# Performance work log

Measured on AMD Instinct MI355X. Metric: run time of the kernel, lower is better.

## Reference

```python
import jax, jax.numpy as jnp
import numpy as np

B, S, D_IN, D_OUT = 4, 2048, 1024, 1024

def setup_inputs() -> dict:
    key = jax.random.key(0)
    k1, k2, k3, k4 = jax.random.split(key, 4)
    sc = 0.02
    return {
        "x": jax.random.normal(k1, (B, S, D_IN), dtype=jnp.float32),
        "Wq": jax.random.normal(k2, (D_OUT, D_IN), dtype=jnp.float32) * sc,
        "Wk": jax.random.normal(k3, (D_OUT, D_IN), dtype=jnp.float32) * sc,
        "Wv": jax.random.normal(k4, (D_OUT, D_IN), dtype=jnp.float32) * sc,
    }

def reference(x, Wq, Wk, Wv):
    # torch Linear: y = x @ W.T  (weights stored [out, in])
    b, n, _ = x.shape
    q = jnp.einsum('bnd,od->bno', x, Wq)  # [B,S,D_OUT]
    k = jnp.einsum('bnd,od->bno', x, Wk)
    v = jnp.einsum('bnd,od->bno', x, Wv)
    scores = jnp.einsum('bqd,bkd->bqk', q, k)  # [B,S,S]
    # causal mask: positions j > i masked to -inf BEFORE scaling (matches source)
    causal = jnp.triu(jnp.ones((n, n), dtype=bool), k=1)
    scores = jnp.where(causal[None, :, :], -jnp.inf, scores)
    scale = 1.0 / jnp.sqrt(jnp.float32(k.shape[-1]))
    attn = jax.nn.softmax(scores * scale, axis=-1)
    # NOTE: source calls dropout but discards its output -> no-op
    return jnp.einsum('bqk,bkd->bqd', attn, v)
```

## Files before the change

### kernel.cpp

```cpp
#include <hip/hip_runtime.h>
#include <hip/hip_bf16.h>
#include <hip/hip_fp16.h>


using bf16 = __hip_bfloat16;
typedef __bf16 bf16x8 __attribute__((ext_vector_type(8)));
typedef float f32x4 __attribute__((ext_vector_type(4)));

__device__ __forceinline__ void load_lds_16B(const void* g, void* l) {
  __builtin_amdgcn_global_load_lds(
      (const __attribute__((address_space(1))) unsigned int*)g,
      (__attribute__((address_space(3))) unsigned int*)l, 16, 0, 0);
}

template <int N>
__device__ __forceinline__ void waitcnt_vm() {
  if constexpr (N == 8) asm volatile("s_waitcnt vmcnt(8)" ::: "memory");
  else if constexpr (N == 6) asm volatile("s_waitcnt vmcnt(6)" ::: "memory");
  else if constexpr (N == 4) asm volatile("s_waitcnt vmcnt(4)" ::: "memory");
  else if constexpr (N == 3) asm volatile("s_waitcnt vmcnt(3)" ::: "memory");
  else asm volatile("s_waitcnt vmcnt(0)" ::: "memory");
}

__device__ __forceinline__ int swz(int o) { return o ^ (((o >> 7) & 7) << 4); }

template <int M_REP, bool OUT_BF16, bool CSKIP, bool KLIM>
__global__ __launch_bounds__(512, 2) void gemm_pipe(
    const bf16* __restrict__ A, const bf16* __restrict__ Bm, void* __restrict__ Cv,
    int M, int N, int K, long sAz, long sBz, long sCzBytes) {
  constexpr int BM = M_REP * 32;
  constexpr int BN = 256;
  constexpr int ABYT = BM * 64;
  constexpr int BBYT = BN * 64;
  constexpr int NCALL = (ABYT + BBYT) / 8192;

  const int tn = blockIdx.x, tm = blockIdx.y, z = blockIdx.z;
  if (CSKIP && tn * BN >= tm * BM + BM) return;
  A += (long)z * sAz;
  Bm += (long)z * sBz;
  char* C = (char*)Cv + (long)z * sCzBytes;

  int kEnd = K;
  if (KLIM) kEnd = min(tm * BM + BM, K);
  const int nt = kEnd >> 5;

  __shared__ char sm[4 * (ABYT + BBYT)];

  const int tid = threadIdx.x;
  const int lane = tid & 63, wv = tid >> 6;
  const int wr = wv >> 2, wc = wv & 3;

  const char* srcp[NCALL];
  int ldsbase[NCALL];
  int bufstride[NCALL];
#pragma unroll
  for (int c = 0; c < NCALL; c++) {
    int oall = c * 8192 + tid * 16;
    int oc = c * 8192 + wv * 1024;
    bool isB = oall >= ABYT;
    int toff = isB ? (oall - ABYT) : oall;
    int os = swz(toff);
    int row = os >> 6, colb = os & 63;
    const bf16* rowp = isB ? (Bm + (long)(tn * BN + row) * K)
                           : (A + (long)(tm * BM + row) * K);
    srcp[c] = (const char*)rowp + colb;
    ldsbase[c] = isB ? (4 * ABYT + (oc - ABYT)) : oc;
    bufstride[c] = isB ? BBYT : ABYT;
  }
  auto stage = [&](int tt) {
#pragma unroll
    for (int c = 0; c < NCALL; c++)
      load_lds_16B(srcp[c] + (long)tt * 64, sm + ldsbase[c] + (tt & 3) * bufstride[c]);
  };

  int aoff[M_REP], boff[4];
#pragma unroll
  for (int m = 0; m < M_REP; m++) {
    int row = wr * (M_REP * 16) + m * 16 + (lane & 15);
    aoff[m] = swz(row * 64 + (lane >> 4) * 16);
  }
#pragma unroll
  for (int n = 0; n < 4; n++) {
    int row = wc * 64 + n * 16 + (lane & 15);
    boff[n] = swz(row * 64 + (lane >> 4) * 16) + 4 * ABYT;
  }

  f32x4 acc[M_REP][4] = {};

  if (nt > 0) stage(0);
  if (nt > 1) stage(1);
  if (nt > 2) stage(2);

  for (int t = 0; t < nt; t++) {
    if (t + 3 <= nt) waitcnt_vm<2 * NCALL>();
    else if (t + 2 == nt) waitcnt_vm<NCALL>();
    else waitcnt_vm<0>();
    __builtin_amdgcn_s_barrier();

    const int buf = t & 3;
    bf16x8 bfr[4], afr[M_REP];
#pragma unroll
    for (int n = 0; n < 4; n++)
      bfr[n] = *(const bf16x8*)(sm + boff[n] + buf * BBYT);
#pragma unroll
    for (int m = 0; m < M_REP; m++)
      afr[m] = *(const bf16x8*)(sm + aoff[m] + buf * ABYT);

    if (t + 3 < nt) stage(t + 3);

    __builtin_amdgcn_s_setprio(1);
#pragma unroll
    for (int m = 0; m < M_REP; m++)
#pragma unroll
      for (int n = 0; n < 4; n++)
        acc[m][n] = __builtin_amdgcn_mfma_f32_16x16x32_bf16(afr[m], bfr[n], acc[m][n], 0, 0, 0);
    __builtin_amdgcn_s_setprio(0);
  }

  const int cr0 = tm * BM + wr * (M_REP * 16) + (lane >> 4) * 4;
  const int cc0 = tn * BN + wc * 64 + (lane & 15);
#pragma unroll
  for (int m = 0; m < M_REP; m++)
#pragma unroll
    for (int n = 0; n < 4; n++)
#pragma unroll
      for (int j = 0; j < 4; j++) {
        long row = cr0 + m * 16 + j;
        long col = cc0 + n * 16;
        if (OUT_BF16)
          ((bf16*)C)[row * (long)N + col] = __float2bfloat16(acc[m][n][j]);
        else
          ((float*)C)[row * (long)N + col] = acc[m][n][j];
      }
}

__global__ __launch_bounds__(256) void cvt4(const float* __restrict__ src,
                                            bf16* __restrict__ dst, int n4) {
  int i = blockIdx.x * 256 + threadIdx.x;
  if (i >= n4) return;
  float4 f = ((const float4*)src)[i];
  union {
    bf16 b[4];
    uint2 u;
  } o;
  o.b[0] = __float2bfloat16(f.x);
  o.b[1] = __float2bfloat16(f.y);
  o.b[2] = __float2bfloat16(f.z);
  o.b[3] = __float2bfloat16(f.w);
  ((uint2*)dst)[i] = o.u;
}

__global__ __launch_bounds__(256) void softmax_causal(const float* __restrict__ Sc,
                                                      bf16* __restrict__ P) {
  const int i = blockIdx.x;
  const int b = blockIdx.y;
  const long base = ((long)b * 2048 + i) * 2048;
  const float* row = Sc + base;
  bf16* prow = P + base;
  const int tid = threadIdx.x;
  const int lane = tid & 63, wv = tid >> 6;
  const int len = i + 1;

  float v[8];
#pragma unroll
  for (int u = 0; u < 8; u++) {
    int j = tid + u * 256;
    v[u] = (j < len) ? row[j] : -3.3e38f;
  }
  float m = v[0];
#pragma unroll
  for (int u = 1; u < 8; u++) m = fmaxf(m, v[u]);
  for (int o = 32; o; o >>= 1) m = fmaxf(m, __shfl_xor(m, o));
  __shared__ float redm[4];
  __shared__ float reds[4];
  if (lane == 0) redm[wv] = m;
  __syncthreads();
  m = fmaxf(fmaxf(redm[0], redm[1]), fmaxf(redm[2], redm[3]));

  const float scale = 0.03125f;
  float e[8];
  float s = 0.f;
#pragma unroll
  for (int u = 0; u < 8; u++) {
    int j = tid + u * 256;
    float t = (j < len) ? __expf((v[u] - m) * scale) : 0.f;
    e[u] = t;
    s += t;
  }
  for (int o = 32; o; o >>= 1) s += __shfl_xor(s, o);
  if (lane == 0) reds[wv] = s;
  __syncthreads();
  s = reds[0] + reds[1] + reds[2] + reds[3];
  float inv = 1.0f / s;
#pragma unroll
  for (int u = 0; u < 8; u++) {
    int j = tid + u * 256;
    prow[j] = __float2bfloat16(e[u] * inv);
  }
}

__global__ __launch_bounds__(256) void transposeV(const bf16* __restrict__ V,
                                                  bf16* __restrict__ Vt) {
  __shared__ bf16 t[32][33];
  const int b = blockIdx.z;
  const int s0 = blockIdx.x << 5;
  const int d0 = blockIdx.y << 5;
  const bf16* Vb = V + (long)b * 2048 * 1024;
  bf16* Vtb = Vt + (long)b * 1024 * 2048;
  const int lx = threadIdx.x & 31, ly = threadIdx.x >> 5;
#pragma unroll
  for (int r = 0; r < 32; r += 8)
    t[r + ly][lx] = Vb[(long)(s0 + r + ly) * 1024 + d0 + lx];
  __syncthreads();
#pragma unroll
  for (int r = 0; r < 32; r += 8)
    Vtb[(long)(d0 + r + ly) * 2048 + s0 + lx] = t[lx][r + ly];
}

extern "C" void kernel_launch(void* const* d_in, const int* in_sizes, int n_in,
                              void* d_out, int out_size, void* d_ws, size_t ws_size,
                              hipStream_t stream) {
  const float* x = (const float*)d_in[0];
  const float* Wq = (const float*)d_in[1];
  const float* Wk = (const float*)d_in[2];
  const float* Wv = (const float*)d_in[3];

  const long MBy = 1 << 20;
  char* ws = (char*)d_ws;
  bf16* Q = (bf16*)(ws);
  bf16* Kb = (bf16*)(ws + 16 * MBy);
  bf16* V = (bf16*)(ws + 32 * MBy);
  bf16* Vt = (bf16*)(ws + 48 * MBy);
  bf16* P = (bf16*)(ws + 64 * MBy);
  float* Sc = (float*)(ws + 96 * MBy);
  bf16* xb = (bf16*)(ws + 96 * MBy);
  bf16* Wb = (bf16*)(ws + 112 * MBy);

  cvt4<<<8192, 256, 0, stream>>>(x, xb, 2097152);
  cvt4<<<1024, 256, 0, stream>>>(Wq, Wb, 262144);
  cvt4<<<1024, 256, 0, stream>>>(Wk, Wb + 1048576, 262144);
  cvt4<<<1024, 256, 0, stream>>>(Wv, Wb + 2097152, 262144);

  gemm_pipe<4, true, false, false><<<dim3(4, 64, 3), 512, 0, stream>>>(
      xb, Wb, Q, 8192, 1024, 1024, 0L, 1048576L, 16 * MBy);

  gemm_pipe<8, false, true, false><<<dim3(8, 8, 4), 512, 0, stream>>>(
      Q, Kb, Sc, 2048, 2048, 1024, 2048L * 1024, 2048L * 1024, 2048L * 2048 * 4);

  softmax_causal<<<dim3(2048, 4), 256, 0, stream>>>(Sc, P);

  transposeV<<<dim3(64, 32, 4), 256, 0, stream>>>(V, Vt);

  gemm_pipe<4, false, false, true><<<dim3(4, 16, 4), 512, 0, stream>>>(
      P, Vt, d_out, 2048, 1024, 2048, 2048L * 2048, 1024L * 2048, 2048L * 1024 * 4);
}
```

Measured before the change: 182.3 us.

## Rewrite GEMM as 8-phase double-buffered K=64 pipeline and vectorize softmax

Replaces the 4-stage K=32 GEMM pipeline with a double-buffered K=64 schedule. Each K chunk is split into eight phases that interleave LDS fragment reads, global-to-LDS staging and MFMA bursts, separated by barriers. The QKV projection now uses 256-row tiles, and the four conversion launches are merged into one kernel. Softmax switches to float4 loads and packed bf16 stores, and the V transpose moves earlier in the launch order. The extra barriers and hand-written vmcnt counts add synchronization overhead and correctness risk.

```diff
diff --git a/kernel.cpp b/kernel.cpp
--- a/kernel.cpp
+++ b/kernel.cpp
@@ -1,6 +1,5 @@
 #include <hip/hip_runtime.h>
 #include <hip/hip_bf16.h>
-#include <hip/hip_fp16.h>
 
 
 using bf16 = __hip_bfloat16;
@@ -15,107 +14,131 @@
 
 template <int N>
 __device__ __forceinline__ void waitcnt_vm() {
-  if constexpr (N == 8) asm volatile("s_waitcnt vmcnt(8)" ::: "memory");
-  else if constexpr (N == 6) asm volatile("s_waitcnt vmcnt(6)" ::: "memory");
-  else if constexpr (N == 4) asm volatile("s_waitcnt vmcnt(4)" ::: "memory");
-  else if constexpr (N == 3) asm volatile("s_waitcnt vmcnt(3)" ::: "memory");
+  if constexpr (N == 6) asm volatile("s_waitcnt vmcnt(6)" ::: "memory");
+  else if constexpr (N == 5) asm volatile("s_waitcnt vmcnt(5)" ::: "memory");
   else asm volatile("s_waitcnt vmcnt(0)" ::: "memory");
 }
 
 __device__ __forceinline__ int swz(int o) { return o ^ (((o >> 7) & 7) << 4); }
 
 template <int M_REP, bool OUT_BF16, bool CSKIP, bool KLIM>
-__global__ __launch_bounds__(512, 2) void gemm_pipe(
+__global__ __launch_bounds__(512, 2) void gemm8p(
     const bf16* __restrict__ A, const bf16* __restrict__ Bm, void* __restrict__ Cv,
     int M, int N, int K, long sAz, long sBz, long sCzBytes) {
-  constexpr int BM = M_REP * 32;
-  constexpr int BN = 256;
-  constexpr int ABYT = BM * 64;
-  constexpr int BBYT = BN * 64;
-  constexpr int NCALL = (ABYT + BBYT) / 8192;
+  constexpr int BM = M_REP * 32, BN = 256;
+  constexpr int MH2 = M_REP / 2;
+  constexpr int AKC = BM * 64;
+  constexpr int BKC = BN * 64;
+  constexpr int DBSTR = 2 * AKC + 2 * BKC;
+  constexpr int ACALLS = AKC / 8192;
+  constexpr int VM_LEAVE = ACALLS + 4;
 
   const int tn = blockIdx.x, tm = blockIdx.y, z = blockIdx.z;
-  if (CSKIP && tn * BN >= tm * BM + BM) return;
+  if (CSKIP && tn > tm) return;
   A += (long)z * sAz;
   Bm += (long)z * sBz;
   char* C = (char*)Cv + (long)z * sCzBytes;
 
   int kEnd = K;
   if (KLIM) kEnd = min(tm * BM + BM, K);
-  const int nt = kEnd >> 5;
-
-  __shared__ char sm[4 * (ABYT + BBYT)];
-
-  const int tid = threadIdx.x;
-  const int lane = tid & 63, wv = tid >> 6;
+  const int nt = kEnd >> 6;
+  const int NI = nt >> 1;
+
+  __shared__ __align__(128) char sm[2 * DBSTR];
+  const int tid = threadIdx.x, lane = tid & 63, wv = tid >> 6;
   const int wr = wv >> 2, wc = wv & 3;
-
-  const char* srcp[NCALL];
-  int ldsbase[NCALL];
-  int bufstride[NCALL];
-#pragma unroll
-  for (int c = 0; c < NCALL; c++) {
-    int oall = c * 8192 + tid * 16;
-    int oc = c * 8192 + wv * 1024;
-    bool isB = oall >= ABYT;
-    int toff = isB ? (oall - ABYT) : oall;
-    int os = swz(toff);
-    int row = os >> 6, colb = os & 63;
-    const bf16* rowp = isB ? (Bm + (long)(tn * BN + row) * K)
-                           : (A + (long)(tm * BM + row) * K);
-    srcp[c] = (const char*)rowp + colb;
-    ldsbase[c] = isB ? (4 * ABYT + (oc - ABYT)) : oc;
-    bufstride[c] = isB ? BBYT : ABYT;
-  }
-  auto stage = [&](int tt) {
-#pragma unroll
-    for (int c = 0; c < NCALL; c++)
-      load_lds_16B(srcp[c] + (long)tt * 64, sm + ldsbase[c] + (tt & 3) * bufstride[c]);
+  const int ldsw = wv * 1024;
+
+  const char* srcA[ACALLS];
+  const char* srcB[2];
+#pragma unroll
+  for (int c = 0; c < ACALLS; c++) {
+    int os = swz(c * 8192 + tid * 16);
+    srcA[c] = (const char*)(A + ((long)tm * BM + (os >> 6)) * K) + (os & 63);
+  }
+#pragma unroll
+  for (int c = 0; c < 2; c++) {
+    int os = swz(c * 8192 + tid * 16);
+    srcB[c] = (const char*)(Bm + ((long)tn * BN + (os >> 6)) * K) + (os & 63);
+  }
+  auto stageA = [&](int t, int kc) {
+#pragma unroll
+    for (int c = 0; c < ACALLS; c++)
+      load_lds_16B(srcA[c] + (long)t * 128 + kc * 64,
+                   sm + (t & 1) * DBSTR + kc * AKC + c * 8192 + ldsw);
   };
+  auto stageB = [&](int t, int kc) {
+#pragma unroll
+    for (int c = 0; c < 2; c++)
+      load_lds_16B(srcB[c] + (long)t * 128 + kc * 64,
+                   sm + (t & 1) * DBSTR + 2 * AKC + kc * BKC + c * 8192 + ldsw);
+  };
 
   int aoff[M_REP], boff[4];
 #pragma unroll
-  for (int m = 0; m < M_REP; m++) {
-    int row = wr * (M_REP * 16) + m * 16 + (lane & 15);
-    aoff[m] = swz(row * 64 + (lane >> 4) * 16);
-  }
-#pragma unroll
-  for (int n = 0; n < 4; n++) {
-    int row = wc * 64 + n * 16 + (lane & 15);
-    boff[n] = swz(row * 64 + (lane >> 4) * 16) + 4 * ABYT;
-  }
+  for (int m = 0; m < M_REP; m++)
+    aoff[m] = swz((wr * (M_REP * 16) + m * 16 + (lane & 15)) * 64 + (lane >> 4) * 16);
+#pragma unroll
+  for (int n = 0; n < 4; n++)
+    boff[n] = 2 * AKC + swz((wc * 64 + n * 16 + (lane & 15)) * 64 + (lane >> 4) * 16);
 
   f32x4 acc[M_REP][4] = {};
-
-  if (nt > 0) stage(0);
-  if (nt > 1) stage(1);
-  if (nt > 2) stage(2);
-
-  for (int t = 0; t < nt; t++) {
-    if (t + 3 <= nt) waitcnt_vm<2 * NCALL>();
-    else if (t + 2 == nt) waitcnt_vm<NCALL>();
-    else waitcnt_vm<0>();
-    __builtin_amdgcn_s_barrier();
-
-    const int buf = t & 3;
-    bf16x8 bfr[4], afr[M_REP];
-#pragma unroll
-    for (int n = 0; n < 4; n++)
-      bfr[n] = *(const bf16x8*)(sm + boff[n] + buf * BBYT);
-#pragma unroll
-    for (int m = 0; m < M_REP; m++)
-      afr[m] = *(const bf16x8*)(sm + aoff[m] + buf * ABYT);
-
-    if (t + 3 < nt) stage(t + 3);
-
-    __builtin_amdgcn_s_setprio(1);
-#pragma unroll
-    for (int m = 0; m < M_REP; m++)
-#pragma unroll
-      for (int n = 0; n < 4; n++)
-        acc[m][n] = __builtin_amdgcn_mfma_f32_16x16x32_bf16(afr[m], bfr[n], acc[m][n], 0, 0, 0);
-    __builtin_amdgcn_s_setprio(0);
-  }
+  bf16x8 bfr[2][4];
+  bf16x8 afrA[MH2], afrB[MH2];
+
+#define LDB(DBUF, KC)                                                          \
+  _Pragma("unroll") for (int n = 0; n < 4; n++)                                \
+      bfr[KC][n] = *(const bf16x8*)(sm + (DBUF)*DBSTR + (KC)*BKC + boff[n]);
+#define LDA(DBUF, KC, MH, DST)                                                 \
+  _Pragma("unroll") for (int m = 0; m < MH2; m++)                              \
+      DST[m] = *(const bf16x8*)(sm + (DBUF)*DBSTR + (KC)*AKC + aoff[(MH)*MH2 + m]);
+#define MFMAS(KC, MH, AFR)                                                     \
+  __builtin_amdgcn_s_setprio(1);                                               \
+  _Pragma("unroll") for (int m = 0; m < MH2; m++)                              \
+      _Pragma("unroll") for (int n = 0; n < 4; n++)                            \
+          acc[(MH)*MH2 + m][n] = __builtin_amdgcn_mfma_f32_16x16x32_bf16(      \
+              AFR[m], bfr[KC][n], acc[(MH)*MH2 + m][n], 0, 0, 0);              \
+  __builtin_amdgcn_s_setprio(0);
+#define BAR1()                                                                 \
+  __builtin_amdgcn_s_barrier();                                                \
+  asm volatile("s_waitcnt lgkmcnt(0)" ::: "memory");                           \
+  __builtin_amdgcn_sched_barrier(0);
+#define BAR2() __builtin_amdgcn_s_barrier();
+
+  stageB(0, 0); stageA(0, 0); stageB(0, 1); stageA(0, 1);
+  stageB(1, 0); stageA(1, 0); stageB(1, 1);
+  waitcnt_vm<VM_LEAVE>();
+  __builtin_amdgcn_s_barrier();
+
+  for (int i = 0; i < NI - 1; i++) {
+    const int ta = 2 * i, tb = 2 * i + 1;
+    LDB(0, 0); LDA(0, 0, 0, afrA); stageA(tb, 1);     BAR1(); MFMAS(0, 0, afrA); BAR2();
+    LDA(0, 0, 1, afrB);            stageB(ta + 2, 0); BAR1(); MFMAS(0, 1, afrB); BAR2();
+    LDB(0, 1); LDA(0, 1, 0, afrA); stageA(ta + 2, 0); BAR1(); MFMAS(1, 0, afrA); BAR2();
+    LDA(0, 1, 1, afrB);            stageB(ta + 2, 1);
+    waitcnt_vm<VM_LEAVE>();                           BAR1(); MFMAS(1, 1, afrB); BAR2();
+    LDB(1, 0); LDA(1, 0, 0, afrA); stageA(ta + 2, 1); BAR1(); MFMAS(0, 0, afrA); BAR2();
+    LDA(1, 0, 1, afrB);            stageB(tb + 2, 0); BAR1(); MFMAS(0, 1, afrB); BAR2();
+    LDB(1, 1); LDA(1, 1, 0, afrA); stageA(tb + 2, 0); BAR1(); MFMAS(1, 0, afrA); BAR2();
+    LDA(1, 1, 1, afrB);            stageB(tb + 2, 1);
+    waitcnt_vm<VM_LEAVE>();                           BAR1(); MFMAS(1, 1, afrB); BAR2();
+  }
+  {
+    const int tb = nt - 1;
+    LDB(0, 0); LDA(0, 0, 0, afrA); stageA(tb, 1); BAR1(); MFMAS(0, 0, afrA); BAR2();
+    LDA(0, 0, 1, afrB);                           BAR1(); MFMAS(0, 1, afrB); BAR2();
+    LDB(0, 1); LDA(0, 1, 0, afrA);                BAR1(); MFMAS(1, 0, afrA); BAR2();
+    LDA(0, 1, 1, afrB); waitcnt_vm<0>();          BAR1(); MFMAS(1, 1, afrB); BAR2();
+    LDB(1, 0); LDA(1, 0, 0, afrA);                BAR1(); MFMAS(0, 0, afrA); BAR2();
+    LDA(1, 0, 1, afrB);                           BAR1(); MFMAS(0, 1, afrB); BAR2();
+    LDB(1, 1); LDA(1, 1, 0, afrA);                BAR1(); MFMAS(1, 0, afrA); BAR2();
+    LDA(1, 1, 1, afrB);                           BAR1(); MFMAS(1, 1, afrB); BAR2();
+  }
+#undef LDB
+#undef LDA
+#undef MFMAS
+#undef BAR1
+#undef BAR2
 
   const int cr0 = tm * BM + wr * (M_REP * 16) + (lane >> 4) * 4;
   const int cc0 = tn * BN + wc * 64 + (lane & 15);
@@ -134,68 +157,83 @@
       }
 }
 
-__global__ __launch_bounds__(256) void cvt4(const float* __restrict__ src,
-                                            bf16* __restrict__ dst, int n4) {
-  int i = blockIdx.x * 256 + threadIdx.x;
-  if (i >= n4) return;
+__global__ __launch_bounds__(256) void cvt_all(const float* __restrict__ x,
+                                               const float* __restrict__ wq,
+                                               const float* __restrict__ wk,
+                                               const float* __restrict__ wv,
+                                               bf16* __restrict__ xb,
+                                               bf16* __restrict__ wb) {
+  const int b = blockIdx.x;
+  const float* src;
+  bf16* dst;
+  int i;
+  if (b < 8192) { src = x; dst = xb; i = b * 256 + threadIdx.x; }
+  else if (b < 9216) { src = wq; dst = wb; i = (b - 8192) * 256 + threadIdx.x; }
+  else if (b < 10240) { src = wk; dst = wb + 1048576; i = (b - 9216) * 256 + threadIdx.x; }
+  else { src = wv; dst = wb + 2097152; i = (b - 10240) * 256 + threadIdx.x; }
   float4 f = ((const float4*)src)[i];
-  union {
-    bf16 b[4];
-    uint2 u;
-  } o;
-  o.b[0] = __float2bfloat16(f.x);
-  o.b[1] = __float2bfloat16(f.y);
-  o.b[2] = __float2bfloat16(f.z);
-  o.b[3] = __float2bfloat16(f.w);
+  union { bf16 h[4]; uint2 u; } o;
+  o.h[0] = __float2bfloat16(f.x);
+  o.h[1] = __float2bfloat16(f.y);
+  o.h[2] = __float2bfloat16(f.z);
+  o.h[3] = __float2bfloat16(f.w);
   ((uint2*)dst)[i] = o.u;
 }
 
 __global__ __launch_bounds__(256) void softmax_causal(const float* __restrict__ Sc,
                                                       bf16* __restrict__ P) {
-  const int i = blockIdx.x;
-  const int b = blockIdx.y;
+  const int i = blockIdx.x, b = blockIdx.y;
   const long base = ((long)b * 2048 + i) * 2048;
-  const float* row = Sc + base;
+  const float4* row4 = (const float4*)(Sc + base);
   bf16* prow = P + base;
-  const int tid = threadIdx.x;
-  const int lane = tid & 63, wv = tid >> 6;
+  const int tid = threadIdx.x, lane = tid & 63, wv = tid >> 6;
   const int len = i + 1;
 
   float v[8];
-#pragma unroll
-  for (int u = 0; u < 8; u++) {
-    int j = tid + u * 256;
-    v[u] = (j < len) ? row[j] : -3.3e38f;
-  }
-  float m = v[0];
-#pragma unroll
-  for (int u = 1; u < 8; u++) m = fmaxf(m, v[u]);
+  float m = -3.3e38f;
+#pragma unroll
+  for (int u = 0; u < 2; u++) {
+    float4 f = row4[tid + u * 256];
+    int j0 = (tid + u * 256) * 4;
+    float* pv = v + u * 4;
+    pv[0] = f.x; pv[1] = f.y; pv[2] = f.z; pv[3] = f.w;
+#pragma unroll
+    for (int e = 0; e < 4; e++) {
+      if (j0 + e >= len) pv[e] = -3.3e38f;
+      m = fmaxf(m, pv[e]);
+    }
+  }
   for (int o = 32; o; o >>= 1) m = fmaxf(m, __shfl_xor(m, o));
-  __shared__ float redm[4];
-  __shared__ float reds[4];
+  __shared__ float redm[4], reds[4];
   if (lane == 0) redm[wv] = m;
   __syncthreads();
   m = fmaxf(fmaxf(redm[0], redm[1]), fmaxf(redm[2], redm[3]));
 
   const float scale = 0.03125f;
-  float e[8];
+  float e8[8];
   float s = 0.f;
 #pragma unroll
-  for (int u = 0; u < 8; u++) {
-    int j = tid + u * 256;
-    float t = (j < len) ? __expf((v[u] - m) * scale) : 0.f;
-    e[u] = t;
-    s += t;
+  for (int u = 0; u < 2; u++) {
+    int j0 = (tid + u * 256) * 4;
+#pragma unroll
+    for (int e = 0; e < 4; e++) {
+      float t = (j0 + e < len) ? __expf((v[u * 4 + e] - m) * scale) : 0.f;
+      e8[u * 4 + e] = t;
+      s += t;
+    }
   }
   for (int o = 32; o; o >>= 1) s += __shfl_xor(s, o);
   if (lane == 0) reds[wv] = s;
   __syncthreads();
   s = reds[0] + reds[1] + reds[2] + reds[3];
-  float inv = 1.0f / s;
-#pragma unroll
-  for (int u = 0; u < 8; u++) {
-    int j = tid + u * 256;
-    prow[j] = __float2bfloat16(e[u] * inv);
+  const float inv = 1.0f / s;
+#pragma unroll
+  for (int u = 0; u < 2; u++) {
+    int j0 = (tid + u * 256) * 4;
+    union { bf16 h[4]; uint2 u2; } o;
+#pragma unroll
+    for (int e = 0; e < 4; e++) o.h[e] = __float2bfloat16(e8[u * 4 + e] * inv);
+    *(uint2*)(prow + j0) = o.u2;
   }
 }
 
@@ -236,21 +274,18 @@
   bf16* xb = (bf16*)(ws + 96 * MBy);
   bf16* Wb = (bf16*)(ws + 112 * MBy);
 
-  cvt4<<<8192, 256, 0, stream>>>(x, xb, 2097152);
-  cvt4<<<1024, 256, 0, stream>>>(Wq, Wb, 262144);
-  cvt4<<<1024, 256, 0, stream>>>(Wk, Wb + 1048576, 262144);
-  cvt4<<<1024, 256, 0, stream>>>(Wv, Wb + 2097152, 262144);
-
-  gemm_pipe<4, true, false, false><<<dim3(4, 64, 3), 512, 0, stream>>>(
+  cvt_all<<<11264, 256, 0, stream>>>(x, Wq, Wk, Wv, xb, Wb);
+
+  gemm8p<8, true, false, false><<<dim3(4, 32, 3), 512, 0, stream>>>(
       xb, Wb, Q, 8192, 1024, 1024, 0L, 1048576L, 16 * MBy);
 
-  gemm_pipe<8, false, true, false><<<dim3(8, 8, 4), 512, 0, stream>>>(
+  transposeV<<<dim3(64, 32, 4), 256, 0, stream>>>(V, Vt);
+
+  gemm8p<8, false, true, false><<<dim3(8, 8, 4), 512, 0, stream>>>(
       Q, Kb, Sc, 2048, 2048, 1024, 2048L * 1024, 2048L * 1024, 2048L * 2048 * 4);
 
   softmax_causal<<<dim3(2048, 4), 256, 0, stream>>>(Sc, P);
 
-  transposeV<<<dim3(64, 32, 4), 256, 0, stream>>>(V, Vt);
-
-  gemm_pipe<4, false, false, true><<<dim3(4, 16, 4), 512, 0, stream>>>(
+  gemm8p<4, false, false, true><<<dim3(4, 16, 4), 512, 0, stream>>>(
       P, Vt, d_out, 2048, 1024, 2048, 2048L * 2048, 1024L * 2048, 2048L * 1024 * 4);
 }
```

After: 169.4 us. -7.1%, faster.
